# Optimization experiments

Measured on AMD Instinct MI355X. Metric: run time of the kernel, lower is better.

The kernel has to match this reference:

```python
import jax, jax.numpy as jnp
import numpy as np

INPUTDIM = 256
OUTDIM = 256
GRIDSIZE = 300


def setup_inputs() -> dict:
    key = jax.random.key(0)
    k1, k2 = jax.random.split(key)
    x = jax.random.normal(k1, (1024, INPUTDIM), dtype=jnp.float32)
    scale = 1.0 / (np.sqrt(INPUTDIM) * np.sqrt(GRIDSIZE))
    fouriercoeffs = jax.random.normal(k2, (2, OUTDIM, INPUTDIM, GRIDSIZE), dtype=jnp.float32) * scale
    bias = jnp.zeros((1, OUTDIM), dtype=jnp.float32)
    return {"x": x, "fouriercoeffs": fouriercoeffs, "bias": bias}


def reference(x, fouriercoeffs, bias):
    # x: (B, I); fouriercoeffs: (2, O, I, G); bias: (1, O)
    outshape = x.shape[:-1] + (OUTDIM,)
    xf = x.reshape(-1, INPUTDIM)
    k = jnp.arange(1, GRIDSIZE + 1, dtype=xf.dtype)  # (G,)
    phase = xf[:, :, None] * k[None, None, :]        # (B, I, G)
    c = jnp.cos(phase)
    s = jnp.sin(phase)
    y = jnp.einsum('big,jig->bj', c, fouriercoeffs[0]) \
        + jnp.einsum('big,jig->bj', s, fouriercoeffs[1])
    y = y + bias
    return y.reshape(outshape)
```

## Files before the change

kernel.cpp:

```cpp
#include <hip/hip_runtime.h>

#define BATCH   1024
#define IDIM    256
#define ODIM    256
#define GRIDSZ  300
#define KS_     64
#define IPW     4
#define CHUNKS  19
#define NSTEPS  (IPW * CHUNKS)
#define INV2PI  0.15915494309189535f

typedef __attribute__((ext_vector_type(8))) short  short8;
typedef __attribute__((ext_vector_type(4))) float  f32x4;
typedef __attribute__((ext_vector_type(4))) unsigned int u32x4;

__device__ __forceinline__ unsigned pk(float c, float s) {
  unsigned a = __float_as_uint(c) + 0x8000u;
  unsigned b = __float_as_uint(s) + 0x8000u;
  return __builtin_amdgcn_perm(b, a, 0x07060302u);
}

__device__ __forceinline__ void dma16(const float* g, const float* l) {
  __builtin_amdgcn_global_load_lds(
      (const __attribute__((address_space(1))) unsigned int*)(g),
      (__attribute__((address_space(3))) unsigned int*)(l), 16, 0, 0);
}

__device__ __forceinline__ void rot(float& c, float& s, float C, float S) {
  float t1 = s * S, t2 = c * S;
  float cn = __builtin_fmaf(c, C, -t1);
  s = __builtin_fmaf(s, C, t2);
  c = cn;
}

__device__ __forceinline__ void cossin(float rev, float& c, float& s) {
  c = __builtin_amdgcn_cosf(__builtin_amdgcn_fractf(rev));
  s = __builtin_amdgcn_cosf(__builtin_amdgcn_fractf(rev - 0.25f));
}

__global__ void init_out(const float* __restrict__ bias, float* __restrict__ out) {
  const int idx = blockIdx.x * 256 + threadIdx.x;
  out[idx] = bias[idx & (ODIM - 1)];
}

__global__ __launch_bounds__(256, 4) void fkan_dma(
    const float* __restrict__ x, const float* __restrict__ fc,
    float* __restrict__ out) {
  __shared__ alignas(16) unsigned int Bp[2][1024];
  __shared__ alignas(16) float Bf[2048];

  const int tid = threadIdx.x, id = blockIdx.x;
  const int z = id & 7;
  const int m = (id >> 3) & 3;
  const int nk = (id >> 5) * 8 + z;
  const int n  = nk & 3;
  const int ks = nk >> 2;

  const int wave = tid >> 6, lane = tid & 63;
  const int fr = lane & 15, fq = lane >> 4;
  const int mbase = m * 256 + wave * 64;
  const int nbase = n * 64;

  f32x4 acc[4][4];
#pragma unroll
  for (int a_ = 0; a_ < 4; ++a_)
#pragma unroll
    for (int b_ = 0; b_ < 4; ++b_)
      acc[a_][b_] = (f32x4){0.f, 0.f, 0.f, 0.f};

  float r1c[4], r1s[4], r16c[4], r16s[4], sc_[4], ss_[4];

  const float* b1 = fc + (size_t)ODIM * IDIM * GRIDSZ;

  int fo = ((nbase + wave * 16 + fr) * IDIM + ks * IPW) * GRIDSZ + fq * 4;
  const int sa = wave * 256 + lane * 4;
  const float* myBf0 = &Bf[sa];
  const float* myBf1 = &Bf[1024 + sa];

  dma16(fc + fo, myBf0);
  dma16(b1 + fo, myBf1);
  asm volatile("s_waitcnt vmcnt(0)" ::: "memory");
  {
    const f32x4 La = *(const f32x4*)myBf0;
    const f32x4 Lb = *(const f32x4*)myBf1;
    *(u32x4*)&Bp[0][sa] =
        (u32x4){pk(La.x, Lb.x), pk(La.y, Lb.y), pk(La.z, Lb.z), pk(La.w, Lb.w)};
  }

  int gs = 0, il = 0;

#pragma unroll 2
  for (int S = 0; S < NSTEPS; ++S) {
    __syncthreads();

    bool zpad = false;
    if (S < NSTEPS - 1) {
      int cg = gs + 1;
      if (cg == CHUNKS) { cg = 0; fo += GRIDSZ - (CHUNKS - 1) * 16; }
      else fo += 16;
      zpad = (cg == CHUNKS - 1) & (fq == 3);
      const int sub = zpad ? 4 : 0;
      dma16(fc + fo - sub, myBf0);
      dma16(b1 + fo - sub, myBf1);
    }

    if (gs == 0) {
      const int i = ks * IPW + il;
#pragma unroll
      for (int tI = 0; tI < 4; ++tI) {
        const float xr = x[(size_t)(mbase + tI * 16 + fr) * IDIM + i] * INV2PI;
        cossin(xr, r1c[tI], r1s[tI]);
        cossin(16.0f * xr, r16c[tI], r16s[tI]);
        cossin((float)(fq * 4 + 1) * xr, sc_[tI], ss_[tI]);
      }
    }

    const unsigned int* buf = &Bp[S & 1][0];
    short8 bV0 = __builtin_bit_cast(short8, *(const u32x4*)(buf + lane * 4));
    short8 bV1 = __builtin_bit_cast(short8, *(const u32x4*)(buf + 256 + lane * 4));
    short8 bV2 = __builtin_bit_cast(short8, *(const u32x4*)(buf + 512 + lane * 4));
    short8 bV3 = __builtin_bit_cast(short8, *(const u32x4*)(buf + 768 + lane * 4));

#pragma unroll
    for (int tI = 0; tI < 4; ++tI) {
      float c = sc_[tI], s = ss_[tI];
      unsigned a0 = pk(c, s);
      rot(c, s, r1c[tI], r1s[tI]); unsigned a1 = pk(c, s);
      rot(c, s, r1c[tI], r1s[tI]); unsigned a2 = pk(c, s);
      rot(c, s, r1c[tI], r1s[tI]); unsigned a3 = pk(c, s);
      rot(sc_[tI], ss_[tI], r16c[tI], r16s[tI]);
      short8 aV = __builtin_bit_cast(short8, (u32x4){a0, a1, a2, a3});
      acc[tI][0] = __builtin_amdgcn_mfma_f32_16x16x32_bf16(aV, bV0, acc[tI][0], 0, 0, 0);
      acc[tI][1] = __builtin_amdgcn_mfma_f32_16x16x32_bf16(aV, bV1, acc[tI][1], 0, 0, 0);
      acc[tI][2] = __builtin_amdgcn_mfma_f32_16x16x32_bf16(aV, bV2, acc[tI][2], 0, 0, 0);
      acc[tI][3] = __builtin_amdgcn_mfma_f32_16x16x32_bf16(aV, bV3, acc[tI][3], 0, 0, 0);
    }

    if (S < NSTEPS - 1) {
      asm volatile("s_waitcnt vmcnt(0)" ::: "memory");
      const f32x4 La = *(const f32x4*)myBf0;
      const f32x4 Lb = *(const f32x4*)myBf1;
      u32x4 w = (u32x4){pk(La.x, Lb.x), pk(La.y, Lb.y),
                        pk(La.z, Lb.z), pk(La.w, Lb.w)};
      if (zpad) w = (u32x4){0u, 0u, 0u, 0u};
      *(u32x4*)&Bp[(S + 1) & 1][sa] = w;
    }

    gs++; if (gs == CHUNKS) { gs = 0; ++il; }
  }

  const int ob = mbase + fq * 4;
  const int oj = nbase + fr;
#pragma unroll
  for (int tI = 0; tI < 4; ++tI)
#pragma unroll
    for (int tJ = 0; tJ < 4; ++tJ) {
      float* dst = out + (size_t)(ob + tI * 16) * ODIM + (oj + tJ * 16);
#pragma unroll
      for (int rr = 0; rr < 4; ++rr)
        unsafeAtomicAdd(dst + rr * ODIM, acc[tI][tJ][rr]);
    }
}

extern "C" void kernel_launch(void* const* d_in, const int* in_sizes, int n_in,
                              void* d_out, int out_size, void* d_ws, size_t ws_size,
                              hipStream_t stream) {
  const float* x    = (const float*)d_in[0];
  const float* fc   = (const float*)d_in[1];
  const float* bias = (const float*)d_in[2];
  float* out = (float*)d_out;

  init_out<<<dim3(BATCH * ODIM / 256), dim3(256), 0, stream>>>(bias, out);
  fkan_dma<<<dim3(4 * 4 * KS_), dim3(256), 0, stream>>>(x, fc, out);
}
```

Measured before the change: 326.5 us.

## Double-buffer the fp32 DMA staging so coefficient loads run two steps ahead

The single fp32 LDS staging buffer becomes two buffers, and global_load_lds prefetch now runs two chunks ahead instead of one. The padding flag is carried across iterations to match the new prefetch distance. The loop-top __syncthreads is replaced with an explicit lgkmcnt wait plus s_barrier between sched_barriers, and the per-step wait uses vmcnt(2) so the newest prefetch can stay in flight. The aim is to hide more global-memory latency behind the MFMA work. The cost is extra LDS per block and more fragile index and wait-count bookkeeping.

```diff
diff --git a/kernel.cpp b/kernel.cpp
--- a/kernel.cpp
+++ b/kernel.cpp
@@ -43,11 +43,11 @@
   out[idx] = bias[idx & (ODIM - 1)];
 }
 
-__global__ __launch_bounds__(256, 4) void fkan_dma(
+__global__ __launch_bounds__(256, 4) void fkan_pipe(
     const float* __restrict__ x, const float* __restrict__ fc,
     float* __restrict__ out) {
   __shared__ alignas(16) unsigned int Bp[2][1024];
-  __shared__ alignas(16) float Bf[2048];
+  __shared__ alignas(16) float Bf[2][2048];
 
   const int tid = threadIdx.x, id = blockIdx.x;
   const int z = id & 7;
@@ -74,35 +74,31 @@
 
   int fo = ((nbase + wave * 16 + fr) * IDIM + ks * IPW) * GRIDSZ + fq * 4;
   const int sa = wave * 256 + lane * 4;
-  const float* myBf0 = &Bf[sa];
-  const float* myBf1 = &Bf[1024 + sa];
 
-  dma16(fc + fo, myBf0);
-  dma16(b1 + fo, myBf1);
-  asm volatile("s_waitcnt vmcnt(0)" ::: "memory");
+  dma16(fc + fo, &Bf[0][sa]);
+  dma16(b1 + fo, &Bf[0][1024 + sa]);
+  fo += 16;
+  dma16(fc + fo, &Bf[1][sa]);
+  dma16(b1 + fo, &Bf[1][1024 + sa]);
+
+  asm volatile("s_waitcnt vmcnt(2)" ::: "memory");
   {
-    const f32x4 La = *(const f32x4*)myBf0;
-    const f32x4 Lb = *(const f32x4*)myBf1;
+    const f32x4 La = *(const f32x4*)&Bf[0][sa];
+    const f32x4 Lb = *(const f32x4*)&Bf[0][1024 + sa];
     *(u32x4*)&Bp[0][sa] =
         (u32x4){pk(La.x, Lb.x), pk(La.y, Lb.y), pk(La.z, Lb.z), pk(La.w, Lb.w)};
   }
 
   int gs = 0, il = 0;
+  int gd = 2;
+  bool zpA = false;
 
 #pragma unroll 2
   for (int S = 0; S < NSTEPS; ++S) {
-    __syncthreads();
-
-    bool zpad = false;
-    if (S < NSTEPS - 1) {
-      int cg = gs + 1;
-      if (cg == CHUNKS) { cg = 0; fo += GRIDSZ - (CHUNKS - 1) * 16; }
-      else fo += 16;
-      zpad = (cg == CHUNKS - 1) & (fq == 3);
-      const int sub = zpad ? 4 : 0;
-      dma16(fc + fo - sub, myBf0);
-      dma16(b1 + fo - sub, myBf1);
-    }
+    __builtin_amdgcn_sched_barrier(0);
+    asm volatile("s_waitcnt lgkmcnt(0)" ::: "memory");
+    __builtin_amdgcn_s_barrier();
+    __builtin_amdgcn_sched_barrier(0);
 
     if (gs == 0) {
       const int i = ks * IPW + il;
@@ -113,6 +109,17 @@
         cossin(16.0f * xr, r16c[tI], r16s[tI]);
         cossin((float)(fq * 4 + 1) * xr, sc_[tI], ss_[tI]);
       }
+    }
+
+    bool zpB = false;
+    if (S < NSTEPS - 2) {
+      if (gd == 0) fo += GRIDSZ - (CHUNKS - 1) * 16;
+      else fo += 16;
+      zpB = (gd == CHUNKS - 1) & (fq == 3);
+      const int sub = zpB ? 4 : 0;
+      dma16(fc + fo - sub, &Bf[S & 1][sa]);
+      dma16(b1 + fo - sub, &Bf[S & 1][1024 + sa]);
+      gd++; if (gd == CHUNKS) gd = 0;
     }
 
     const unsigned int* buf = &Bp[S & 1][0];
@@ -137,15 +144,19 @@
     }
 
     if (S < NSTEPS - 1) {
-      asm volatile("s_waitcnt vmcnt(0)" ::: "memory");
-      const f32x4 La = *(const f32x4*)myBf0;
-      const f32x4 Lb = *(const f32x4*)myBf1;
+      if (S < NSTEPS - 2) {
+        asm volatile("s_waitcnt vmcnt(2)" ::: "memory");
+      } else {
+        asm volatile("s_waitcnt vmcnt(0)" ::: "memory");
+      }
+      const f32x4 La = *(const f32x4*)&Bf[(S + 1) & 1][sa];
+      const f32x4 Lb = *(const f32x4*)&Bf[(S + 1) & 1][1024 + sa];
       u32x4 w = (u32x4){pk(La.x, Lb.x), pk(La.y, Lb.y),
                         pk(La.z, Lb.z), pk(La.w, Lb.w)};
-      if (zpad) w = (u32x4){0u, 0u, 0u, 0u};
+      if (zpA) w = (u32x4){0u, 0u, 0u, 0u};
       *(u32x4*)&Bp[(S + 1) & 1][sa] = w;
     }
-
+    zpA = zpB;
     gs++; if (gs == CHUNKS) { gs = 0; ++il; }
   }
 
@@ -171,5 +182,5 @@
   float* out = (float*)d_out;
 
   init_out<<<dim3(BATCH * ODIM / 256), dim3(256), 0, stream>>>(bias, out);
-  fkan_dma<<<dim3(4 * 4 * KS_), dim3(256), 0, stream>>>(x, fc, out);
+  fkan_pipe<<<dim3(4 * 4 * KS_), dim3(256), 0, stream>>>(x, fc, out);
 }
```

Result: no change. 322.2 us (-1.3%).
